# Kernel optimization log

Measured on AMD Instinct MI355X. Metric: run time of the kernel, lower is better.

Reference implementation:

```python
import jax, jax.numpy as jnp
import numpy as np


def setup_inputs() -> dict:
    key = jax.random.key(0)
    ks = jax.random.split(key, 6)
    B, Nab, Nag, d, K = 16, 16384, 16384, 128, 10
    return {
        "H1": jax.random.normal(ks[0], (B, Nab, d), jnp.float32),
        "H2": jax.random.normal(ks[1], (B, Nag, d), jnp.float32),
        "X1": jax.random.normal(ks[2], (B, Nab, 3), jnp.float32),
        "X2": jax.random.normal(ks[3], (B, Nag, 3), jnp.float32),
        "W1": jax.random.uniform(ks[4], (K, d, d), jnp.float32),
        "W2": jax.random.uniform(ks[5], (K, d, d), jnp.float32),
    }


def _kabsch(P, Q):
    # Rigid alignment: find R (3x3), t (3,) s.t. P @ R + t ~= Q (least squares).
    c1 = P.mean(axis=0)
    c2 = Q.mean(axis=0)
    Pc = P - c1
    Qc = Q - c2
    Hm = Pc.T @ Qc  # [3,3] covariance
    U, S, Vt = jnp.linalg.svd(Hm, full_matrices=False)
    sign = jnp.sign(jnp.linalg.det(U @ Vt))
    Dm = jnp.diag(jnp.concatenate([jnp.ones(2, dtype=P.dtype), sign[None]]))
    R = U @ Dm @ Vt
    t = c2 - c1 @ R
    return P @ R + t, R, t


def reference(H1, H2, X1, X2, W1, W2):
    # Keypoint cross-attention. Faithful to torch:
    #   alpha_1k = softmax( (H1 @ W1_k @ H2.T).mean(dim=1) / sqrt(d) )
    # Using mean-over-columns identity: (H1 @ W @ H2.T).mean(1) = H1 @ W @ mean(H2,0)
    d = H1.shape[-1]
    scale = 1.0 / np.sqrt(d)
    h2bar = H2.mean(axis=1)  # [B, d]
    h1bar = H1.mean(axis=1)  # [B, d]
    v1 = jnp.einsum('kde,be->bkd', W1, h2bar)          # W1_k @ mean(H2)
    s1 = jnp.einsum('bnd,bkd->bkn', H1, v1) * scale     # [B, K, Nab]
    a1 = jax.nn.softmax(s1, axis=-1)
    Y1 = jnp.einsum('bkn,bnc->bkc', a1, X1)             # [B, K, 3]
    v2 = jnp.einsum('kde,be->bkd', W2, h1bar)
    s2 = jnp.einsum('bmd,bkd->bkm', H2, v2) * scale     # [B, K, Nag]
    a2 = jax.nn.softmax(s2, axis=-1)
    Y2 = jnp.einsum('bkm,bmc->bkc', a2, X2)             # [B, K, 3]
    Y1_aligned, R, t = jax.vmap(_kabsch)(Y1, Y2)
    return jnp.stack([Y1, Y2, Y1_aligned], axis=1)      # [B, 3, K, 3]
```

## Files before the change

kernel.cpp:

```cpp
#include <hip/hip_runtime.h>
#include <math.h>

#define NB 16
#define NN 16384
#define DD 128
#define KK 10

#define WS_FLOATS 46336

__device__ __forceinline__ float4 f4add(float4 a, float4 b) {
    return make_float4(a.x + b.x, a.y + b.y, a.z + b.z, a.w + b.w);
}

__global__ __launch_bounds__(256, 8) void k_sum(const float* __restrict__ H,
                                                float* __restrict__ dst) {
    int bi = blockIdx.x;
    int b = bi >> 8;
    int chunk = bi & 255;
    const float4* src4 = (const float4*)(H + ((size_t)b * NN + (size_t)chunk * 64) * DD);
    int tid = threadIdx.x;
    float4 x0 = src4[0 * 256 + tid];
    float4 x1 = src4[1 * 256 + tid];
    float4 x2 = src4[2 * 256 + tid];
    float4 x3 = src4[3 * 256 + tid];
    float4 x4 = src4[4 * 256 + tid];
    float4 x5 = src4[5 * 256 + tid];
    float4 x6 = src4[6 * 256 + tid];
    float4 x7 = src4[7 * 256 + tid];
    float4 a = f4add(f4add(f4add(x0, x1), f4add(x2, x3)),
                     f4add(f4add(x4, x5), f4add(x6, x7)));
    a.x += __shfl_xor(a.x, 32);
    a.y += __shfl_xor(a.y, 32);
    a.z += __shfl_xor(a.z, 32);
    a.w += __shfl_xor(a.w, 32);
    __shared__ float red[4][32][4];
    int wv = tid >> 6, lane = tid & 63;
    if (lane < 32) {
        red[wv][lane][0] = a.x; red[wv][lane][1] = a.y;
        red[wv][lane][2] = a.z; red[wv][lane][3] = a.w;
    }
    __syncthreads();
    if (tid < 32) {
        float t0 = 0.f, t1 = 0.f, t2 = 0.f, t3 = 0.f;
#pragma unroll
        for (int w = 0; w < 4; ++w) {
            t0 += red[w][tid][0]; t1 += red[w][tid][1];
            t2 += red[w][tid][2]; t3 += red[w][tid][3];
        }
        float* d = dst + (size_t)b * DD + tid * 4;
        atomicAdd(d + 0, t0);
        atomicAdd(d + 1, t1);
        atomicAdd(d + 2, t2);
        atomicAdd(d + 3, t3);
    }
}

__global__ __launch_bounds__(128) void k_v(const float* __restrict__ W,
                                           const float* __restrict__ hsrc,
                                           float* __restrict__ vdst) {
    int bi = blockIdx.x;
    int b = bi / 10;
    int k = bi % 10;
    const float* Wk = W + (size_t)k * DD * DD;
    const float* hb = hsrc + (size_t)b * DD;
    __shared__ float4 h_s[32];
    int tid = threadIdx.x;
    if (tid < 32) h_s[tid] = ((const float4*)hb)[tid];
    __syncthreads();
    const float4* Wrow = (const float4*)(Wk + (size_t)tid * DD);
    float acc = 0.f;
#pragma unroll 8
    for (int e4 = 0; e4 < 32; ++e4) {
        float4 w4 = Wrow[e4];
        float4 h4 = h_s[e4];
        acc += w4.x * h4.x + w4.y * h4.y + w4.z * h4.z + w4.w * h4.w;
    }
    const float SCALE = (float)(1.0 / (16384.0 * 11.313708498984761));
    vdst[((size_t)b * KK + k) * DD + tid] = acc * SCALE;
}

template <bool FOLD>
__global__ __launch_bounds__(256) void k_scores(const float* __restrict__ H,
                                                const float* __restrict__ X,
                                                const float* __restrict__ v,
                                                float* __restrict__ accgp,
                                                float* __restrict__ hsum0) {
    int bi = blockIdx.x;
    int b = bi >> 7;
    int tile = bi & 127;
    int row0 = tile << 7;
    const float* Hb = H + (size_t)b * NN * DD;
    const float* Xb = X + (size_t)b * NN * 3;
    const float* vp = v + (size_t)b * KK * DD;

    __shared__ float4 v_s4[KK * DD / 4];
    __shared__ float red[4][40];
    __shared__ float4 colred4[4][2][16];

    int tid = threadIdx.x;
    for (int i = tid; i < KK * DD / 4; i += 256)
        v_s4[i] = ((const float4*)vp)[i];
    __syncthreads();

    int g = tid >> 4;
    int l = tid & 15;
    float kmask = (l < KK) ? 1.f : 0.f;

    float pse = 0.f, py0 = 0.f, py1 = 0.f, py2 = 0.f;
    float4 cs0 = make_float4(0.f, 0.f, 0.f, 0.f);
    float4 cs1 = make_float4(0.f, 0.f, 0.f, 0.f);

    int n0 = row0 + g * 2;
    const float* hp = Hb + (size_t)n0 * DD + (l << 2);
    float4 h00 = *(const float4*)(hp);
    float4 h01 = *(const float4*)(hp + 64);
    float4 h10 = *(const float4*)(hp + DD);
    float4 h11 = *(const float4*)(hp + DD + 64);
    float xa0 = Xb[(size_t)n0 * 3 + 0];
    float xa1 = Xb[(size_t)n0 * 3 + 1];
    float xa2 = Xb[(size_t)n0 * 3 + 2];
    float xb0 = Xb[(size_t)n0 * 3 + 3];
    float xb1 = Xb[(size_t)n0 * 3 + 4];
    float xb2 = Xb[(size_t)n0 * 3 + 5];

#pragma unroll
    for (int sweep = 0; sweep < 4; ++sweep) {
        float4 p00, p01, p10, p11;
        float qa0, qa1, qa2, qb0, qb1, qb2;
        if (sweep < 3) {
            const float* hpn = hp + (size_t)(sweep + 1) * 32 * DD;
            p00 = *(const float4*)(hpn);
            p01 = *(const float4*)(hpn + 64);
            p10 = *(const float4*)(hpn + DD);
            p11 = *(const float4*)(hpn + DD + 64);
            size_t xn = (size_t)(n0 + (sweep + 1) * 32) * 3;
            qa0 = Xb[xn + 0]; qa1 = Xb[xn + 1]; qa2 = Xb[xn + 2];
            qb0 = Xb[xn + 3]; qb1 = Xb[xn + 4]; qb2 = Xb[xn + 5];
        }
        if (FOLD) {
            cs0 = f4add(cs0, f4add(h00, h10));
            cs1 = f4add(cs1, f4add(h01, h11));
        }
        float acc0[KK], acc1[KK];
#pragma unroll
        for (int k = 0; k < KK; ++k) {
            float4 v0 = v_s4[k * 32 + l];
            float4 v1 = v_s4[k * 32 + 16 + l];
            acc0[k] = h00.x * v0.x + h00.y * v0.y + h00.z * v0.z + h00.w * v0.w
                    + h01.x * v1.x + h01.y * v1.y + h01.z * v1.z + h01.w * v1.w;
            acc1[k] = h10.x * v0.x + h10.y * v0.y + h10.z * v0.z + h10.w * v0.w
                    + h11.x * v1.x + h11.y * v1.y + h11.z * v1.z + h11.w * v1.w;
        }
#pragma unroll
        for (int k = 0; k < KK; ++k) {
            float s0 = acc0[k], s1 = acc1[k];
            s0 += __shfl_xor(s0, 1); s0 += __shfl_xor(s0, 2);
            s0 += __shfl_xor(s0, 4); s0 += __shfl_xor(s0, 8);
            s1 += __shfl_xor(s1, 1); s1 += __shfl_xor(s1, 2);
            s1 += __shfl_xor(s1, 4); s1 += __shfl_xor(s1, 8);
            acc0[k] = s0; acc1[k] = s1;
        }
        float u0 = 0.f, u1 = 0.f;
#pragma unroll
        for (int k = 0; k < KK; ++k) {
            if (k == l) { u0 = acc0[k]; u1 = acc1[k]; }
        }
        float e0 = kmask * __expf(u0);
        float e1 = kmask * __expf(u1);
        pse += e0 + e1;
        py0 += e0 * xa0 + e1 * xb0;
        py1 += e0 * xa1 + e1 * xb1;
        py2 += e0 * xa2 + e1 * xb2;
        if (sweep < 3) {
            h00 = p00; h01 = p01; h10 = p10; h11 = p11;
            xa0 = qa0; xa1 = qa1; xa2 = qa2;
            xb0 = qb0; xb1 = qb1; xb2 = qb2;
        }
    }
    pse += __shfl_xor(pse, 16); pse += __shfl_xor(pse, 32);
    py0 += __shfl_xor(py0, 16); py0 += __shfl_xor(py0, 32);
    py1 += __shfl_xor(py1, 16); py1 += __shfl_xor(py1, 32);
    py2 += __shfl_xor(py2, 16); py2 += __shfl_xor(py2, 32);
    if (FOLD) {
        cs0.x += __shfl_xor(cs0.x, 16); cs0.x += __shfl_xor(cs0.x, 32);
        cs0.y += __shfl_xor(cs0.y, 16); cs0.y += __shfl_xor(cs0.y, 32);
        cs0.z += __shfl_xor(cs0.z, 16); cs0.z += __shfl_xor(cs0.z, 32);
        cs0.w += __shfl_xor(cs0.w, 16); cs0.w += __shfl_xor(cs0.w, 32);
        cs1.x += __shfl_xor(cs1.x, 16); cs1.x += __shfl_xor(cs1.x, 32);
        cs1.y += __shfl_xor(cs1.y, 16); cs1.y += __shfl_xor(cs1.y, 32);
        cs1.z += __shfl_xor(cs1.z, 16); cs1.z += __shfl_xor(cs1.z, 32);
        cs1.w += __shfl_xor(cs1.w, 16); cs1.w += __shfl_xor(cs1.w, 32);
    }
    int wv = tid >> 6, lane = tid & 63;
    if (lane < 16) {
        if (lane < KK) {
            red[wv][lane] = pse;
            red[wv][10 + lane] = py0;
            red[wv][20 + lane] = py1;
            red[wv][30 + lane] = py2;
        }
        if (FOLD) {
            colred4[wv][0][lane] = cs0;
            colred4[wv][1][lane] = cs1;
        }
    }
    __syncthreads();
    if (tid < 40) {
        float s = red[0][tid] + red[1][tid] + red[2][tid] + red[3][tid];
        atomicAdd(accgp + (size_t)b * 40 + tid, s);
    }
    if (FOLD && tid < 128) {
        int j = tid >> 6, cc = tid & 63, ll = cc >> 2, c = cc & 3;
        float s = 0.f;
#pragma unroll
        for (int w = 0; w < 4; ++w) s += ((const float*)&colred4[w][j][ll])[c];
        atomicAdd(hsum0 + (size_t)b * DD + tid, s);
    }
}

__global__ __launch_bounds__(64) void k_final(const float* __restrict__ accg,
                                              float* __restrict__ out) {
    int b = blockIdx.x;
    int tid = threadIdx.x;
    __shared__ float Ys[2][KK][3];
    if (tid < 2 * KK * 3) {
        int p = tid / 30;
        int r = tid % 30;
        int k = r / 3;
        int c = r % 3;
        const float* a = accg + (size_t)(p * NB + b) * 40;
        float val = a[10 + c * 10 + k] / a[k];
        Ys[p][k][c] = val;
        out[((size_t)(b * 3 + p) * KK + k) * 3 + c] = val;
    }
    __syncthreads();
    if (tid == 0) {
        double P[KK][3], Q[KK][3];
        double c1[3] = {0, 0, 0}, c2[3] = {0, 0, 0};
        for (int i = 0; i < KK; ++i)
            for (int c = 0; c < 3; ++c) {
                P[i][c] = (double)Ys[0][i][c];
                Q[i][c] = (double)Ys[1][i][c];
                c1[c] += P[i][c];
                c2[c] += Q[i][c];
            }
        for (int c = 0; c < 3; ++c) { c1[c] /= KK; c2[c] /= KK; }
        double A0[3][3];
        for (int a = 0; a < 3; ++a)
            for (int c = 0; c < 3; ++c) {
                double s = 0;
                for (int i = 0; i < KK; ++i) s += (P[i][a] - c1[a]) * (Q[i][c] - c2[c]);
                A0[a][c] = s;
            }
        double Bm[3][3], V[3][3];
        for (int a = 0; a < 3; ++a)
            for (int c = 0; c < 3; ++c) { Bm[a][c] = A0[a][c]; V[a][c] = (a == c) ? 1.0 : 0.0; }
        for (int sweep = 0; sweep < 16; ++sweep)
            for (int p = 0; p < 2; ++p)
                for (int q = p + 1; q < 3; ++q) {
                    double al = 0, be = 0, ga = 0;
                    for (int r = 0; r < 3; ++r) {
                        al += Bm[r][p] * Bm[r][p];
                        be += Bm[r][q] * Bm[r][q];
                        ga += Bm[r][p] * Bm[r][q];
                    }
                    if (fabs(ga) < 1e-300) continue;
                    double zeta = (be - al) / (2.0 * ga);
                    double t = copysign(1.0, zeta) / (fabs(zeta) + sqrt(1.0 + zeta * zeta));
                    double cs = 1.0 / sqrt(1.0 + t * t);
                    double sn = cs * t;
                    for (int r = 0; r < 3; ++r) {
                        double bp = Bm[r][p], bq = Bm[r][q];
                        Bm[r][p] = cs * bp - sn * bq;
                        Bm[r][q] = sn * bp + cs * bq;
                        double vp = V[r][p], vq = V[r][q];
                        V[r][p] = cs * vp - sn * vq;
                        V[r][q] = sn * vp + cs * vq;
                    }
                }
        double sig[3];
        for (int j = 0; j < 3; ++j) {
            sig[j] = sqrt(Bm[0][j] * Bm[0][j] + Bm[1][j] * Bm[1][j] + Bm[2][j] * Bm[2][j]);
            if (sig[j] < 1e-300) sig[j] = 1e-300;
        }
        int jmin = 0;
        if (sig[1] < sig[jmin]) jmin = 1;
        if (sig[2] < sig[jmin]) jmin = 2;
        double det = A0[0][0] * (A0[1][1] * A0[2][2] - A0[1][2] * A0[2][1])
                   - A0[0][1] * (A0[1][0] * A0[2][2] - A0[1][2] * A0[2][0])
                   + A0[0][2] * (A0[1][0] * A0[2][1] - A0[1][1] * A0[2][0]);
        double sgn = (det >= 0.0) ? 1.0 : -1.0;
        double R[3][3];
        for (int a = 0; a < 3; ++a)
            for (int c = 0; c < 3; ++c) {
                double s = 0;
                for (int j = 0; j < 3; ++j) {
                    double dj = (j == jmin) ? sgn : 1.0;
                    s += dj * (Bm[a][j] / sig[j]) * V[c][j];
                }
                R[a][c] = s;
            }
        for (int i = 0; i < KK; ++i)
            for (int c = 0; c < 3; ++c) {
                double s = c2[c];
                for (int a = 0; a < 3; ++a) s += (P[i][a] - c1[a]) * R[a][c];
                out[((size_t)(b * 3 + 2) * KK + i) * 3 + c] = (float)s;
            }
    }
}

extern "C" void kernel_launch(void* const* d_in, const int* in_sizes, int n_in,
                              void* d_out, int out_size, void* d_ws, size_t ws_size,
                              hipStream_t stream) {
    const float* H1 = (const float*)d_in[0];
    const float* H2 = (const float*)d_in[1];
    const float* X1 = (const float*)d_in[2];
    const float* X2 = (const float*)d_in[3];
    const float* W1 = (const float*)d_in[4];
    const float* W2 = (const float*)d_in[5];
    float* out = (float*)d_out;
    float* ws = (float*)d_ws;
    float* hsum = ws;
    float* accg = ws + 4096;
    float* v    = ws + 5376;

    hipMemsetAsync(d_ws, 0, 5376 * sizeof(float), stream);
    hipLaunchKernelGGL(k_sum, dim3(4096), dim3(256), 0, stream, H2, hsum + (size_t)NB * DD);
    hipLaunchKernelGGL(k_v, dim3(160), dim3(128), 0, stream, W1, hsum + (size_t)NB * DD, v);
    hipLaunchKernelGGL((k_scores<true>), dim3(2048), dim3(256), 0, stream,
                       H1, X1, v, accg, hsum);
    hipLaunchKernelGGL(k_v, dim3(160), dim3(128), 0, stream, W2, hsum,
                       v + (size_t)NB * KK * DD);
    hipLaunchKernelGGL((k_scores<false>), dim3(2048), dim3(256), 0, stream,
                       H2, X2, v + (size_t)NB * KK * DD, accg + (size_t)NB * 40,
                       (float*)nullptr);
    hipLaunchKernelGGL(k_final, dim3(16), dim3(64), 0, stream, accg, out);
}
```

Measured before the change: 392.1 us.

## Restructure pipeline: batch H1/H2 sums, merged score pass, atomic-free partials, transpose reduce

The old pipeline summed H2 first and folded the H1 column sums into the first score pass. The new one sums H1 and H2 together in one streaming pass, then runs a single k_v launch for both weights and a single k_scores launch for both sides, which removes the serial dependency between the two score passes. Global atomics and the memset are replaced by per-chunk and per-tile partial buffers that the consumer kernels reduce. The per-k shuffle reduction becomes a transpose-style butterfly that does fewer shuffles. In exchange, H1 is now read twice (once to sum, once to score), which adds about one extra pass over 128 MB in a memory-bound workload.

```diff
diff --git a/kernel.cpp b/kernel.cpp
--- a/kernel.cpp
+++ b/kernel.cpp
@@ -5,39 +5,85 @@
 #define NN 16384
 #define DD 128
 #define KK 10
-
-#define WS_FLOATS 46336
+#define NCHUNK 128
+#define NTILE 128
+
 
 __device__ __forceinline__ float4 f4add(float4 a, float4 b) {
     return make_float4(a.x + b.x, a.y + b.y, a.z + b.z, a.w + b.w);
 }
 
-__global__ __launch_bounds__(256, 8) void k_sum(const float* __restrict__ H,
-                                                float* __restrict__ dst) {
+__device__ __forceinline__ float kreduce16(const float a[KK], int l) {
+    const bool h8 = (l & 8) != 0;
+    const bool h4 = (l & 4) != 0;
+    const bool h2 = (l & 2) != 0;
+    const bool h1 = (l & 1) != 0;
+    float b[8];
+#pragma unroll
+    for (int i = 0; i < 8; ++i) {
+        float give = h8 ? a[i] : ((i < 2) ? a[i + 8] : 0.f);
+        float r = __shfl_xor(give, 8);
+        float keep = h8 ? ((i < 2) ? a[i + 8] : 0.f) : a[i];
+        b[i] = keep + r;
+    }
+    float c[4];
+#pragma unroll
+    for (int i = 0; i < 4; ++i) {
+        float give = h4 ? c[0] * 0.f + b[i] : b[i + 4];
+        give = h4 ? b[i] : b[i + 4];
+        float r = __shfl_xor(give, 4);
+        float keep = h4 ? b[i + 4] : b[i];
+        c[i] = keep + r;
+    }
+    float d2[2];
+#pragma unroll
+    for (int i = 0; i < 2; ++i) {
+        float give = h2 ? c[i] : c[i + 2];
+        float r = __shfl_xor(give, 2);
+        float keep = h2 ? c[i + 2] : c[i];
+        d2[i] = keep + r;
+    }
+    float give = h1 ? d2[0] : d2[1];
+    float r = __shfl_xor(give, 1);
+    float keep = h1 ? d2[1] : d2[0];
+    return keep + r;
+}
+
+__global__ __launch_bounds__(256, 8) void k_sums(const float* __restrict__ H1,
+                                                 const float* __restrict__ H2,
+                                                 float* __restrict__ hpart) {
     int bi = blockIdx.x;
-    int b = bi >> 8;
-    int chunk = bi & 255;
-    const float4* src4 = (const float4*)(H + ((size_t)b * NN + (size_t)chunk * 64) * DD);
+    int t = bi >> 11;
+    int rem = bi & 2047;
+    int b = rem >> 7;
+    int chunk = rem & 127;
+    const float4* src4 = (const float4*)((t ? H2 : H1)
+                         + ((size_t)b * NN + (size_t)chunk * 128) * DD);
     int tid = threadIdx.x;
-    float4 x0 = src4[0 * 256 + tid];
-    float4 x1 = src4[1 * 256 + tid];
-    float4 x2 = src4[2 * 256 + tid];
-    float4 x3 = src4[3 * 256 + tid];
-    float4 x4 = src4[4 * 256 + tid];
-    float4 x5 = src4[5 * 256 + tid];
-    float4 x6 = src4[6 * 256 + tid];
-    float4 x7 = src4[7 * 256 + tid];
-    float4 a = f4add(f4add(f4add(x0, x1), f4add(x2, x3)),
-                     f4add(f4add(x4, x5), f4add(x6, x7)));
-    a.x += __shfl_xor(a.x, 32);
-    a.y += __shfl_xor(a.y, 32);
-    a.z += __shfl_xor(a.z, 32);
-    a.w += __shfl_xor(a.w, 32);
+    float4 s = make_float4(0.f, 0.f, 0.f, 0.f);
+#pragma unroll
+    for (int o = 0; o < 2; ++o) {
+        const float4* base = src4 + o * 2048;
+        float4 x0 = base[0 * 256 + tid];
+        float4 x1 = base[1 * 256 + tid];
+        float4 x2 = base[2 * 256 + tid];
+        float4 x3 = base[3 * 256 + tid];
+        float4 x4 = base[4 * 256 + tid];
+        float4 x5 = base[5 * 256 + tid];
+        float4 x6 = base[6 * 256 + tid];
+        float4 x7 = base[7 * 256 + tid];
+        s = f4add(s, f4add(f4add(f4add(x0, x1), f4add(x2, x3)),
+                           f4add(f4add(x4, x5), f4add(x6, x7))));
+    }
+    s.x += __shfl_xor(s.x, 32);
+    s.y += __shfl_xor(s.y, 32);
+    s.z += __shfl_xor(s.z, 32);
+    s.w += __shfl_xor(s.w, 32);
     __shared__ float red[4][32][4];
     int wv = tid >> 6, lane = tid & 63;
     if (lane < 32) {
-        red[wv][lane][0] = a.x; red[wv][lane][1] = a.y;
-        red[wv][lane][2] = a.z; red[wv][lane][3] = a.w;
+        red[wv][lane][0] = s.x; red[wv][lane][1] = s.y;
+        red[wv][lane][2] = s.z; red[wv][lane][3] = s.w;
     }
     __syncthreads();
     if (tid < 32) {
@@ -47,55 +93,61 @@
             t0 += red[w][tid][0]; t1 += red[w][tid][1];
             t2 += red[w][tid][2]; t3 += red[w][tid][3];
         }
-        float* d = dst + (size_t)b * DD + tid * 4;
-        atomicAdd(d + 0, t0);
-        atomicAdd(d + 1, t1);
-        atomicAdd(d + 2, t2);
-        atomicAdd(d + 3, t3);
-    }
-}
-
-__global__ __launch_bounds__(128) void k_v(const float* __restrict__ W,
-                                           const float* __restrict__ hsrc,
-                                           float* __restrict__ vdst) {
+        *(float4*)(hpart + ((size_t)(t * NB + b) * NCHUNK + chunk) * DD + tid * 4)
+            = make_float4(t0, t1, t2, t3);
+    }
+}
+
+__global__ __launch_bounds__(128) void k_v(const float* __restrict__ W1,
+                                           const float* __restrict__ W2,
+                                           const float* __restrict__ hpart,
+                                           float* __restrict__ v) {
     int bi = blockIdx.x;
-    int b = bi / 10;
-    int k = bi % 10;
-    const float* Wk = W + (size_t)k * DD * DD;
-    const float* hb = hsrc + (size_t)b * DD;
-    __shared__ float4 h_s[32];
+    int p = bi / 160;
+    int rem = bi % 160;
+    int b = rem / 10;
+    int k = rem % 10;
+    const float* W = (p ? W2 : W1) + (size_t)k * DD * DD;
+    int srct = 1 - p;
+    __shared__ __align__(16) float hs[DD];
     int tid = threadIdx.x;
-    if (tid < 32) h_s[tid] = ((const float4*)hb)[tid];
-    __syncthreads();
-    const float4* Wrow = (const float4*)(Wk + (size_t)tid * DD);
+    const float* hp = hpart + (size_t)(srct * NB + b) * NCHUNK * DD + tid;
+    float s = 0.f;
+#pragma unroll 8
+    for (int c = 0; c < NCHUNK; ++c) s += hp[(size_t)c * DD];
+    hs[tid] = s;
+    __syncthreads();
+    const float4* Wrow = (const float4*)(W + (size_t)tid * DD);
+    const float4* h4p = (const float4*)hs;
     float acc = 0.f;
 #pragma unroll 8
     for (int e4 = 0; e4 < 32; ++e4) {
         float4 w4 = Wrow[e4];
-        float4 h4 = h_s[e4];
+        float4 h4 = h4p[e4];
         acc += w4.x * h4.x + w4.y * h4.y + w4.z * h4.z + w4.w * h4.w;
     }
     const float SCALE = (float)(1.0 / (16384.0 * 11.313708498984761));
-    vdst[((size_t)b * KK + k) * DD + tid] = acc * SCALE;
-}
-
-template <bool FOLD>
-__global__ __launch_bounds__(256) void k_scores(const float* __restrict__ H,
-                                                const float* __restrict__ X,
+    v[((size_t)(p * NB + b) * KK + k) * DD + tid] = acc * SCALE;
+}
+
+__global__ __launch_bounds__(256) void k_scores(const float* __restrict__ H1,
+                                                const float* __restrict__ H2,
+                                                const float* __restrict__ X1,
+                                                const float* __restrict__ X2,
                                                 const float* __restrict__ v,
-                                                float* __restrict__ accgp,
-                                                float* __restrict__ hsum0) {
+                                                float* __restrict__ spart) {
     int bi = blockIdx.x;
-    int b = bi >> 7;
-    int tile = bi & 127;
+    int p = bi >> 11;
+    int rem = bi & 2047;
+    int b = rem >> 7;
+    int tile = rem & 127;
     int row0 = tile << 7;
-    const float* Hb = H + (size_t)b * NN * DD;
-    const float* Xb = X + (size_t)b * NN * 3;
-    const float* vp = v + (size_t)b * KK * DD;
+    const float* Hb = (p ? H2 : H1) + (size_t)b * NN * DD;
+    const float* Xb = (p ? X2 : X1) + (size_t)b * NN * 3;
+    const float* vp = v + (size_t)(p * NB + b) * KK * DD;
 
     __shared__ float4 v_s4[KK * DD / 4];
     __shared__ float red[4][40];
-    __shared__ float4 colred4[4][2][16];
 
     int tid = threadIdx.x;
     for (int i = tid; i < KK * DD / 4; i += 256)
@@ -107,8 +159,6 @@
     float kmask = (l < KK) ? 1.f : 0.f;
 
     float pse = 0.f, py0 = 0.f, py1 = 0.f, py2 = 0.f;
-    float4 cs0 = make_float4(0.f, 0.f, 0.f, 0.f);
-    float4 cs1 = make_float4(0.f, 0.f, 0.f, 0.f);
 
     int n0 = row0 + g * 2;
     const float* hp = Hb + (size_t)n0 * DD + (l << 2);
@@ -137,10 +187,6 @@
             qa0 = Xb[xn + 0]; qa1 = Xb[xn + 1]; qa2 = Xb[xn + 2];
             qb0 = Xb[xn + 3]; qb1 = Xb[xn + 4]; qb2 = Xb[xn + 5];
         }
-        if (FOLD) {
-            cs0 = f4add(cs0, f4add(h00, h10));
-            cs1 = f4add(cs1, f4add(h01, h11));
-        }
         float acc0[KK], acc1[KK];
 #pragma unroll
         for (int k = 0; k < KK; ++k) {
@@ -151,22 +197,10 @@
             acc1[k] = h10.x * v0.x + h10.y * v0.y + h10.z * v0.z + h10.w * v0.w
                     + h11.x * v1.x + h11.y * v1.y + h11.z * v1.z + h11.w * v1.w;
         }
-#pragma unroll
-        for (int k = 0; k < KK; ++k) {
-            float s0 = acc0[k], s1 = acc1[k];
-            s0 += __shfl_xor(s0, 1); s0 += __shfl_xor(s0, 2);
-            s0 += __shfl_xor(s0, 4); s0 += __shfl_xor(s0, 8);
-            s1 += __shfl_xor(s1, 1); s1 += __shfl_xor(s1, 2);
-            s1 += __shfl_xor(s1, 4); s1 += __shfl_xor(s1, 8);
-            acc0[k] = s0; acc1[k] = s1;
-        }
-        float u0 = 0.f, u1 = 0.f;
-#pragma unroll
-        for (int k = 0; k < KK; ++k) {
-            if (k == l) { u0 = acc0[k]; u1 = acc1[k]; }
-        }
-        float e0 = kmask * __expf(u0);
-        float e1 = kmask * __expf(u1);
+        float s0 = kreduce16(acc0, l);
+        float s1 = kreduce16(acc1, l);
+        float e0 = kmask * __expf(s0);
+        float e1 = kmask * __expf(s1);
         pse += e0 + e1;
         py0 += e0 * xa0 + e1 * xb0;
         py1 += e0 * xa1 + e1 * xb1;
@@ -181,55 +215,40 @@
     py0 += __shfl_xor(py0, 16); py0 += __shfl_xor(py0, 32);
     py1 += __shfl_xor(py1, 16); py1 += __shfl_xor(py1, 32);
     py2 += __shfl_xor(py2, 16); py2 += __shfl_xor(py2, 32);
-    if (FOLD) {
-        cs0.x += __shfl_xor(cs0.x, 16); cs0.x += __shfl_xor(cs0.x, 32);
-        cs0.y += __shfl_xor(cs0.y, 16); cs0.y += __shfl_xor(cs0.y, 32);
-        cs0.z += __shfl_xor(cs0.z, 16); cs0.z += __shfl_xor(cs0.z, 32);
-        cs0.w += __shfl_xor(cs0.w, 16); cs0.w += __shfl_xor(cs0.w, 32);
-        cs1.x += __shfl_xor(cs1.x, 16); cs1.x += __shfl_xor(cs1.x, 32);
-        cs1.y += __shfl_xor(cs1.y, 16); cs1.y += __shfl_xor(cs1.y, 32);
-        cs1.z += __shfl_xor(cs1.z, 16); cs1.z += __shfl_xor(cs1.z, 32);
-        cs1.w += __shfl_xor(cs1.w, 16); cs1.w += __shfl_xor(cs1.w, 32);
-    }
     int wv = tid >> 6, lane = tid & 63;
-    if (lane < 16) {
-        if (lane < KK) {
-            red[wv][lane] = pse;
-            red[wv][10 + lane] = py0;
-            red[wv][20 + lane] = py1;
-            red[wv][30 + lane] = py2;
-        }
-        if (FOLD) {
-            colred4[wv][0][lane] = cs0;
-            colred4[wv][1][lane] = cs1;
-        }
+    if (lane < KK) {
+        red[wv][lane] = pse;
+        red[wv][10 + lane] = py0;
+        red[wv][20 + lane] = py1;
+        red[wv][30 + lane] = py2;
     }
     __syncthreads();
     if (tid < 40) {
         float s = red[0][tid] + red[1][tid] + red[2][tid] + red[3][tid];
-        atomicAdd(accgp + (size_t)b * 40 + tid, s);
-    }
-    if (FOLD && tid < 128) {
-        int j = tid >> 6, cc = tid & 63, ll = cc >> 2, c = cc & 3;
-        float s = 0.f;
-#pragma unroll
-        for (int w = 0; w < 4; ++w) s += ((const float*)&colred4[w][j][ll])[c];
-        atomicAdd(hsum0 + (size_t)b * DD + tid, s);
-    }
-}
-
-__global__ __launch_bounds__(64) void k_final(const float* __restrict__ accg,
-                                              float* __restrict__ out) {
+        spart[((size_t)(p * NB + b) * NTILE + tile) * 40 + tid] = s;
+    }
+}
+
+__global__ __launch_bounds__(128) void k_final(const float* __restrict__ spart,
+                                               float* __restrict__ out) {
     int b = blockIdx.x;
     int tid = threadIdx.x;
+    __shared__ float acc[2][40];
+    if (tid < 80) {
+        int p = tid / 40, j = tid % 40;
+        const float* sp = spart + (size_t)(p * NB + b) * NTILE * 40 + j;
+        float s = 0.f;
+        for (int tile = 0; tile < NTILE; ++tile) s += sp[(size_t)tile * 40];
+        acc[p][j] = s;
+    }
+    __syncthreads();
     __shared__ float Ys[2][KK][3];
     if (tid < 2 * KK * 3) {
         int p = tid / 30;
         int r = tid % 30;
         int k = r / 3;
         int c = r % 3;
-        const float* a = accg + (size_t)(p * NB + b) * 40;
-        float val = a[10 + c * 10 + k] / a[k];
+        float val = acc[p][10 + c * 10 + k] / acc[p][k];
         Ys[p][k][c] = val;
         out[((size_t)(b * 3 + p) * KK + k) * 3 + c] = val;
     }
@@ -320,19 +339,12 @@
     const float* W2 = (const float*)d_in[5];
     float* out = (float*)d_out;
     float* ws = (float*)d_ws;
-    float* hsum = ws;
-    float* accg = ws + 4096;
-    float* v    = ws + 5376;
-
-    hipMemsetAsync(d_ws, 0, 5376 * sizeof(float), stream);
-    hipLaunchKernelGGL(k_sum, dim3(4096), dim3(256), 0, stream, H2, hsum + (size_t)NB * DD);
-    hipLaunchKernelGGL(k_v, dim3(160), dim3(128), 0, stream, W1, hsum + (size_t)NB * DD, v);
-    hipLaunchKernelGGL((k_scores<true>), dim3(2048), dim3(256), 0, stream,
-                       H1, X1, v, accg, hsum);
-    hipLaunchKernelGGL(k_v, dim3(160), dim3(128), 0, stream, W2, hsum,
-                       v + (size_t)NB * KK * DD);
-    hipLaunchKernelGGL((k_scores<false>), dim3(2048), dim3(256), 0, stream,
-                       H2, X2, v + (size_t)NB * KK * DD, accg + (size_t)NB * 40,
-                       (float*)nullptr);
-    hipLaunchKernelGGL(k_final, dim3(16), dim3(64), 0, stream, accg, out);
-}
+    float* hpart = ws;
+    float* v     = ws + 524288;
+    float* spart = ws + 565248;
+
+    hipLaunchKernelGGL(k_sums,   dim3(4096), dim3(256), 0, stream, H1, H2, hpart);
+    hipLaunchKernelGGL(k_v,      dim3(320),  dim3(128), 0, stream, W1, W2, hpart, v);
+    hipLaunchKernelGGL(k_scores, dim3(4096), dim3(256), 0, stream, H1, H2, X1, X2, v, spart);
+    hipLaunchKernelGGL(k_final,  dim3(16),   dim3(128), 0, stream, spart, out);
+}
```

After: 367.4 us. -6.3%, faster.
